# Kernel tuning notes

Measured on AMD Instinct MI355X. Metric: run time of the kernel, lower is better.

The kernel has to match this reference:

```python
import jax, jax.numpy as jnp
import numpy as np

B, S, D, L, H = 4, 2048, 1024, 2, 8  # batch, seq, d_model, hierarchy levels, heads
DH = D // H


def _ln(x, g, b, eps=1e-5):
    mu = jnp.mean(x, axis=-1, keepdims=True)
    xc = x - mu
    var = jnp.mean(xc * xc, axis=-1, keepdims=True)
    return xc * jax.lax.rsqrt(var + eps) * g + b


def setup_inputs() -> dict:
    key = jax.random.key(0)
    ks = jax.random.split(key, 16)
    s = 0.02
    f32 = jnp.float32
    return {
        "x": jax.random.normal(ks[0], (B, S, D), f32),
        "hierarchy_levels": jax.random.randint(ks[1], (B, S), 0, 3),
        # per-level processor MLPs (stacked over level axis)
        "p1_w": jax.random.normal(ks[2], (L, D, D), f32) * s,
        "p1_b": jnp.zeros((L, D), f32),
        "p2_w": jax.random.normal(ks[3], (L, D, D), f32) * s,
        "p2_b": jnp.zeros((L, D), f32),
        "ln_g": jnp.ones((L, D), f32),
        "ln_b": jnp.zeros((L, D), f32),
        # multihead attention projections
        "wq": jax.random.normal(ks[4], (D, D), f32) * s,
        "bq": jnp.zeros((D,), f32),
        "wk": jax.random.normal(ks[5], (D, D), f32) * s,
        "bk": jnp.zeros((D,), f32),
        "wv": jax.random.normal(ks[6], (D, D), f32) * s,
        "bv": jnp.zeros((D,), f32),
        "wo": jax.random.normal(ks[7], (D, D), f32) * s,
        "bo": jnp.zeros((D,), f32),
        # integration MLP: Linear(L*D -> D), SiLU, Linear(D -> D), LayerNorm
        "i1_w": jax.random.normal(ks[8], (L * D, D), f32) * s,
        "i1_b": jnp.zeros((D,), f32),
        "i2_w": jax.random.normal(ks[9], (D, D), f32) * s,
        "i2_b": jnp.zeros((D,), f32),
        "iln_g": jnp.ones((D,), f32),
        "iln_b": jnp.zeros((D,), f32),
    }


def reference(x, hierarchy_levels, p1_w, p1_b, p2_w, p2_b, ln_g, ln_b,
              wq, bq, wk, bk, wv, bv, wo, bo,
              i1_w, i1_b, i2_w, i2_b, iln_g, iln_b):
    # --- per-token expert routing: compute all L processors, select by level ---
    t = jax.nn.silu(jnp.einsum('bsd,lde->lbse', x, p1_w) + p1_b[:, None, None, :])
    h = jnp.einsum('lbse,led->lbsd', t, p2_w) + p2_b[:, None, None, :]
    h = _ln(h, ln_g[:, None, None, :], ln_b[:, None, None, :])  # [L,B,S,D]
    oh = jax.nn.one_hot(hierarchy_levels, L, dtype=x.dtype)      # [B,S,L]; level>=L -> all-zero row
    hsel = jnp.einsum('lbsd,bsl->bsd', h, oh)                    # [B,S,D]
    # --- self-attention over routed outputs ---
    q = (hsel @ wq + bq).reshape(B, S, H, DH)
    k = (hsel @ wk + bk).reshape(B, S, H, DH)
    v = (hsel @ wv + bv).reshape(B, S, H, DH)
    scores = jnp.einsum('bqhd,bkhd->bhqk', q, k) / np.sqrt(DH).astype(x.dtype)
    a = jax.nn.softmax(scores, axis=-1)                          # [B,H,S,S]
    ctx = jnp.einsum('bhqk,bkhd->bqhd', a, v).reshape(B, S, D)
    attended = ctx @ wo + bo
    attn_weights = jnp.mean(a, axis=1)                           # torch avg over heads: [B,S,S]
    # --- integration MLP ---
    z = jnp.concatenate([hsel, attended], axis=-1)               # [B,S,2D]
    z = jax.nn.silu(z @ i1_w + i1_b) @ i2_w + i2_b
    out = _ln(z, iln_g, iln_b)
    return out, attn_weights
```

## Files before the change

### kernel.cpp

```cpp
#include <hip/hip_runtime.h>
#include <cstdint>
#include <cstddef>

#define B_ 4
#define S_ 2048
#define D_ 1024
#define H_ 8
#define DH_ 128
#define MTOT 8192
#define NT_ 32
#define SCALE2 (0.08838834764831845f * 1.4426950408889634f)

typedef __attribute__((ext_vector_type(8))) short s16x8;
typedef __attribute__((ext_vector_type(4))) float f32x4;
typedef __attribute__((ext_vector_type(8))) __bf16 bf16x8;

static __device__ __forceinline__ f32x4 mfma16(s16x8 a, s16x8 b, f32x4 c) {
  return __builtin_amdgcn_mfma_f32_16x16x32_bf16(
      __builtin_bit_cast(bf16x8, a), __builtin_bit_cast(bf16x8, b), c, 0, 0, 0);
}
static __device__ __forceinline__ unsigned short f2bf(float f) {
  unsigned u = __builtin_bit_cast(unsigned, f);
  u += 0x7fffu + ((u >> 16) & 1u);
  return (unsigned short)(u >> 16);
}
static __device__ __forceinline__ float bf2f(unsigned short u) {
  return __builtin_bit_cast(float, (unsigned)u << 16);
}
static __device__ __forceinline__ unsigned cvtpk2(float a, float b) {
  unsigned r;
  asm("v_cvt_pk_bf16_f32 %0, %1, %2" : "=v"(r) : "v"(a), "v"(b));
  return r;
}
static __device__ __forceinline__ void gload_lds16(const void* g, void* l) {
  __builtin_amdgcn_global_load_lds(
      (__attribute__((address_space(1))) void*)(void*)(g),
      (__attribute__((address_space(3))) void*)(l), 16, 0, 0);
}

__global__ __launch_bounds__(256) void xconv_kernel(const float* __restrict__ x,
                                                    unsigned short* __restrict__ xb) {
  long i = ((long)blockIdx.x * 256 + threadIdx.x) * 4;
  float4 v = *(const float4*)(x + i);
  ushort4 o;
  o.x = f2bf(v.x); o.y = f2bf(v.y); o.z = f2bf(v.z); o.w = f2bf(v.w);
  *(ushort4*)(xb + i) = o;
}

__global__ __launch_bounds__(256) void route_kernel(const int* __restrict__ levels,
                                                    int* __restrict__ cnt,
                                                    int* __restrict__ ridx) {
  int row = blockIdx.x * 256 + threadIdx.x;
  int lvl = levels[row];
  if (lvl < 2) {
    int slot = atomicAdd(&cnt[lvl], 1);
    ridx[lvl * MTOT + slot] = row;
  }
}

struct WtDesc { const float* src; unsigned short* dst; long dst_ld; long dst_off; };
struct WtArgs { WtDesc d[10]; };
__global__ __launch_bounds__(256) void wtrans_all_kernel(WtArgs a) {
  __shared__ unsigned short tile[32][33];
  const int wi = blockIdx.y >> 5;
  const WtDesc de = a.d[wi];
  int r0 = (blockIdx.y & 31) * 32, c0 = blockIdx.x * 32;
  int tr = threadIdx.x >> 5, tc = threadIdx.x & 31;
#pragma unroll
  for (int i = 0; i < 4; i++)
    tile[tr + i * 8][tc] = f2bf(de.src[(long)(r0 + tr + i * 8) * 1024 + c0 + tc]);
  __syncthreads();
#pragma unroll
  for (int i = 0; i < 4; i++)
    de.dst[(long)(c0 + tr + i * 8) * de.dst_ld + de.dst_off + r0 + tc] = tile[tc][tr + i * 8];
}

__global__ __launch_bounds__(256) void vtrans_kernel(const unsigned short* __restrict__ V,
                                                     unsigned short* __restrict__ Vt) {
  __shared__ unsigned short tile[32][33];
  int b = blockIdx.z;
  int h = blockIdx.y >> 2, d0 = (blockIdx.y & 3) * 32;
  int s0 = blockIdx.x * 32;
  int tr = threadIdx.x >> 5, tc = threadIdx.x & 31;
#pragma unroll
  for (int i = 0; i < 4; i++)
    tile[tr + i * 8][tc] = V[((long)(b * S_) + s0 + tr + i * 8) * D_ + h * DH_ + d0 + tc];
  __syncthreads();
  const int sk = s0 + tc;
  const int k6 = sk & 63;
  const int slot = ((k6 >> 5) << 5) | (((k6 >> 2) & 3) << 3) | (((k6 >> 4) & 1) << 2) | (k6 & 3);
  const int ss = (sk & ~63) | slot;
#pragma unroll
  for (int i = 0; i < 4; i++)
    Vt[((long)(b * H_ + h) * DH_ + d0 + tr + i * 8) * S_ + ss] = tile[tc][tr + i * 8];
}

template <int TAG>
__global__ __launch_bounds__(256) void gemm_kernel(
    const unsigned short* __restrict__ A, int lda,
    const unsigned short* __restrict__ Wt, int ldw,
    const float* __restrict__ bias, float oscale,
    unsigned short* __restrict__ Cb, float* __restrict__ Cf, int ldc,
    int K, int do_silu) {
  __shared__ unsigned short lA[128 * 64];
  __shared__ unsigned short lB[128 * 64];
  const int t = threadIdx.x;
  const int wid = t >> 6, lane = t & 63;
  const int g = lane >> 4, lc = lane & 15;
  const int wr = wid >> 1, wc = wid & 1;
  const int nwg = gridDim.x * gridDim.y;
  int flat = blockIdx.x + gridDim.x * blockIdx.y;
  flat = (flat & 7) * (nwg >> 3) + (flat >> 3);
  const int m0 = (flat / gridDim.x) * 128;
  const int n0 = (flat % gridDim.x) * 128;
  const int srow = lane >> 3, scol = lane & 7;
  const int sxor = (scol ^ srow) << 4;

  f32x4 acc[4][4];
#pragma unroll
  for (int i = 0; i < 4; i++)
#pragma unroll
    for (int j = 0; j < 4; j++) acc[i][j] = (f32x4){0.f, 0.f, 0.f, 0.f};

  const int nk = K >> 6;
  for (int kt = 0; kt < nk; ++kt) {
    const int k0 = kt << 6;
#pragma unroll
    for (int i = 0; i < 4; i++) {
      const int r0 = wid * 32 + i * 8;
      gload_lds16((const char*)(A + (m0 + r0 + srow) * (long)lda + k0) + sxor,
                  (char*)lA + r0 * 128);
      gload_lds16((const char*)(Wt + (n0 + r0 + srow) * (long)ldw + k0) + sxor,
                  (char*)lB + r0 * 128);
    }
    __syncthreads();
#pragma unroll
    for (int kk = 0; kk < 2; kk++) {
      s16x8 af[4], bfr[4];
#pragma unroll
      for (int i = 0; i < 4; i++) {
        int row = wr * 64 + i * 16 + lc;
        af[i] = *(const s16x8*)((const char*)lA + row * 128 +
                                ((kk * 64 + g * 16) ^ ((row & 7) << 4)));
      }
#pragma unroll
      for (int j = 0; j < 4; j++) {
        int row = wc * 64 + j * 16 + lc;
        bfr[j] = *(const s16x8*)((const char*)lB + row * 128 +
                                 ((kk * 64 + g * 16) ^ ((row & 7) << 4)));
      }
#pragma unroll
      for (int i = 0; i < 4; i++)
#pragma unroll
        for (int j = 0; j < 4; j++) acc[i][j] = mfma16(af[i], bfr[j], acc[i][j]);
    }
    __syncthreads();
  }
#pragma unroll
  for (int i = 0; i < 4; i++) {
    const long rbase = m0 + wr * 64 + i * 16 + g * 4;
#pragma unroll
    for (int j = 0; j < 4; j++) {
      const int col = n0 + wc * 64 + j * 16 + lc;
      const float bv = bias[col];
#pragma unroll
      for (int r = 0; r < 4; r++) {
        float v = (acc[i][j][r] + bv) * oscale;
        if (do_silu) v = v / (1.f + __expf(-v));
        if (Cb) Cb[(rbase + r) * (long)ldc + col] = f2bf(v);
        else Cf[(rbase + r) * (long)ldc + col] = v;
      }
    }
  }
}

template <int TAG>
__global__ __launch_bounds__(512) void gemm8_kernel(
    const unsigned short* __restrict__ A, int lda,
    const unsigned short* __restrict__ Wt, int ldw,
    const float* __restrict__ bias, float oscale,
    unsigned short* __restrict__ Cb, int ldc,
    int K, int do_silu) {
  __shared__ unsigned short lA[128 * 64];
  __shared__ unsigned short lB[128 * 64];
  const int t = threadIdx.x;
  const int wid = t >> 6, lane = t & 63;
  const int g = lane >> 4, lc = lane & 15;
  const int wr = wid >> 1, wc = wid & 1;
  const int nwg = gridDim.x * gridDim.y;
  int flat = blockIdx.x + gridDim.x * blockIdx.y;
  flat = (flat & 7) * (nwg >> 3) + (flat >> 3);
  const int m0 = (flat / gridDim.x) * 128;
  const int n0 = (flat % gridDim.x) * 128;
  const int srow = lane >> 3, scol = lane & 7;
  const int sxor = (scol ^ srow) << 4;

  f32x4 acc[2][4];
#pragma unroll
  for (int i = 0; i < 2; i++)
#pragma unroll
    for (int j = 0; j < 4; j++) acc[i][j] = (f32x4){0.f, 0.f, 0.f, 0.f};

  const int nk = K >> 6;
  for (int kt = 0; kt < nk; ++kt) {
    const int k0 = kt << 6;
#pragma unroll
    for (int i = 0; i < 2; i++) {
      const int r0 = wid * 16 + i * 8;
      gload_lds16((const char*)(A + (m0 + r0 + srow) * (long)lda + k0) + sxor,
                  (char*)lA + r0 * 128);
      gload_lds16((const char*)(Wt + (n0 + r0 + srow) * (long)ldw + k0) + sxor,
                  (char*)lB + r0 * 128);
    }
    __syncthreads();
#pragma unroll
    for (int kk = 0; kk < 2; kk++) {
      s16x8 af[2], bfr[4];
#pragma unroll
      for (int i = 0; i < 2; i++) {
        int row = wr * 32 + i * 16 + lc;
        af[i] = *(const s16x8*)((const char*)lA + row * 128 +
                                ((kk * 64 + g * 16) ^ ((row & 7) << 4)));
      }
#pragma unroll
      for (int j = 0; j < 4; j++) {
        int row = wc * 64 + j * 16 + lc;
        bfr[j] = *(const s16x8*)((const char*)lB + row * 128 +
                                 ((kk * 64 + g * 16) ^ ((row & 7) << 4)));
      }
#pragma unroll
      for (int i = 0; i < 2; i++)
#pragma unroll
        for (int j = 0; j < 4; j++) acc[i][j] = mfma16(af[i], bfr[j], acc[i][j]);
    }
    __syncthreads();
  }
#pragma unroll
  for (int i = 0; i < 2; i++) {
    const long rbase = m0 + wr * 32 + i * 16 + g * 4;
#pragma unroll
    for (int j = 0; j < 4; j++) {
      const int col = n0 + wc * 64 + j * 16 + lc;
      const float bv = bias[col];
#pragma unroll
      for (int r = 0; r < 4; r++) {
        float v = (acc[i][j][r] + bv) * oscale;
        if (do_silu) v = v / (1.f + __expf(-v));
        Cb[(rbase + r) * (long)ldc + col] = f2bf(v);
      }
    }
  }
}

template <int RMAP>
__global__ __launch_bounds__(512) void gemm8_moe_kernel(
    const unsigned short* __restrict__ A, int lda,
    const unsigned short* __restrict__ Wt0, int ldw,
    const float* __restrict__ bias0,
    unsigned short* __restrict__ Cb, int ldc,
    int K, int do_silu, const int* __restrict__ ridx, const int* __restrict__ cnt2) {
  __shared__ unsigned short lA[128 * 64];
  __shared__ unsigned short lB[128 * 64];
  const int t = threadIdx.x;
  const int wid = t >> 6, lane = t & 63;
  const int g = lane >> 4, lc = lane & 15;
  const int wr = wid >> 1, wc = wid & 1;
  const int nwg = gridDim.x * gridDim.y;
  int flat = blockIdx.x + gridDim.x * blockIdx.y;
  flat = (flat & 7) * (nwg >> 3) + (flat >> 3);
  const int m0 = (flat / gridDim.x) * 128;
  const int n0 = (flat % gridDim.x) * 128;
  const int lvl = m0 >> 12;
  const int lm0 = m0 & 4095;
  if (lm0 >= cnt2[lvl]) return;
  const unsigned short* Wt = Wt0 + (long)lvl * 1048576;
  const float* bias = bias0 + lvl * 1024;
  const int srow = lane >> 3, scol = lane & 7;
  const int sxor = (scol ^ srow) << 4;

  const unsigned short* abase[2];
#pragma unroll
  for (int i = 0; i < 2; i++) {
    int ar;
    if (RMAP) ar = ridx[lvl * MTOT + lm0 + wid * 16 + i * 8 + srow];
    else ar = m0 + wid * 16 + i * 8 + srow;
    abase[i] = A + (long)ar * lda;
  }

  f32x4 acc[2][4];
#pragma unroll
  for (int i = 0; i < 2; i++)
#pragma unroll
    for (int j = 0; j < 4; j++) acc[i][j] = (f32x4){0.f, 0.f, 0.f, 0.f};

  const int nk = K >> 6;
  for (int kt = 0; kt < nk; ++kt) {
    const int k0 = kt << 6;
#pragma unroll
    for (int i = 0; i < 2; i++) {
      const int r0 = wid * 16 + i * 8;
      gload_lds16((const char*)(abase[i] + k0) + sxor, (char*)lA + r0 * 128);
      gload_lds16((const char*)(Wt + (n0 + r0 + srow) * (long)ldw + k0) + sxor,
                  (char*)lB + r0 * 128);
    }
    __syncthreads();
#pragma unroll
    for (int kk = 0; kk < 2; kk++) {
      s16x8 af[2], bfr[4];
#pragma unroll
      for (int i = 0; i < 2; i++) {
        int row = wr * 32 + i * 16 + lc;
        af[i] = *(const s16x8*)((const char*)lA + row * 128 +
                                ((kk * 64 + g * 16) ^ ((row & 7) << 4)));
      }
#pragma unroll
      for (int j = 0; j < 4; j++) {
        int row = wc * 64 + j * 16 + lc;
        bfr[j] = *(const s16x8*)((const char*)lB + row * 128 +
                                 ((kk * 64 + g * 16) ^ ((row & 7) << 4)));
      }
#pragma unroll
      for (int i = 0; i < 2; i++)
#pragma unroll
        for (int j = 0; j < 4; j++) acc[i][j] = mfma16(af[i], bfr[j], acc[i][j]);
    }
    __syncthreads();
  }
#pragma unroll
  for (int i = 0; i < 2; i++) {
    const long rbase = m0 + wr * 32 + i * 16 + g * 4;
#pragma unroll
    for (int j = 0; j < 4; j++) {
      const int col = n0 + wc * 64 + j * 16 + lc;
      const float bv = bias[col];
#pragma unroll
      for (int r = 0; r < 4; r++) {
        float v = acc[i][j][r] + bv;
        if (do_silu) v = v / (1.f + __expf(-v));
        Cb[(rbase + r) * (long)ldc + col] = f2bf(v);
      }
    }
  }
}

__global__ __launch_bounds__(256) void wct_gemm_kernel(
    const unsigned short* __restrict__ A,
    const unsigned short* __restrict__ Wb,
    float* __restrict__ Cf) {
  __shared__ unsigned short lA[128 * 64];
  __shared__ unsigned short lB[128 * 64];
  const int t = threadIdx.x;
  const int wid = t >> 6, lane = t & 63;
  const int g = lane >> 4, lc = lane & 15;
  const int wr = wid >> 1, wc = wid & 1;
  const int chunk = blockIdx.y >> 3;
  const int m0 = (blockIdx.y & 7) * 128;
  const int n0 = blockIdx.x * 128;
  const unsigned short* A0 = A + chunk * 256;
  const unsigned short* W0 = Wb + chunk * 256;
  float* C0 = Cf + (long)chunk * 1048576;
  const int srow = lane >> 3, scol = lane & 7;
  const int sxor = (scol ^ srow) << 4;

  f32x4 acc[4][4];
#pragma unroll
  for (int i = 0; i < 4; i++)
#pragma unroll
    for (int j = 0; j < 4; j++) acc[i][j] = (f32x4){0.f, 0.f, 0.f, 0.f};

  for (int kt = 0; kt < 4; ++kt) {
    const int k0 = kt << 6;
#pragma unroll
    for (int i = 0; i < 4; i++) {
      const int r0 = wid * 32 + i * 8;
      gload_lds16((const char*)(A0 + (m0 + r0 + srow) * 2048L + k0) + sxor,
                  (char*)lA + r0 * 128);
      gload_lds16((const char*)(W0 + (n0 + r0 + srow) * 1024L + k0) + sxor,
                  (char*)lB + r0 * 128);
    }
    __syncthreads();
#pragma unroll
    for (int kk = 0; kk < 2; kk++) {
      s16x8 af[4], bfr[4];
#pragma unroll
      for (int i = 0; i < 4; i++) {
        int row = wr * 64 + i * 16 + lc;
        af[i] = *(const s16x8*)((const char*)lA + row * 128 +
                                ((kk * 64 + g * 16) ^ ((row & 7) << 4)));
      }
#pragma unroll
      for (int j = 0; j < 4; j++) {
        int row = wc * 64 + j * 16 + lc;
        bfr[j] = *(const s16x8*)((const char*)lB + row * 128 +
                                 ((kk * 64 + g * 16) ^ ((row & 7) << 4)));
      }
#pragma unroll
      for (int i = 0; i < 4; i++)
#pragma unroll
        for (int j = 0; j < 4; j++) acc[i][j] = mfma16(af[i], bfr[j], acc[i][j]);
    }
    __syncthreads();
  }
#pragma unroll
  for (int i = 0; i < 4; i++) {
    const long rbase = m0 + wr * 64 + i * 16 + g * 4;
#pragma unroll
    for (int j = 0; j < 4; j++) {
      const int col = n0 + wc * 64 + j * 16 + lc;
#pragma unroll
      for (int r = 0; r < 4; r++) C0[(rbase + r) * 1024L + col] = acc[i][j][r];
    }
  }
}

__global__ __launch_bounds__(256) void wct_reduce_kernel(
    const float* __restrict__ hraw, unsigned short* __restrict__ i1t) {
  long e = ((long)blockIdx.x * 256 + threadIdx.x) * 2;
  float a0 = hraw[e] + hraw[e + 1048576] + hraw[e + 2097152] + hraw[e + 3145728];
  float a1 = hraw[e + 1] + hraw[e + 1 + 1048576] + hraw[e + 1 + 2097152] +
             hraw[e + 1 + 3145728];
  unsigned pk = cvtpk2(a0, a1);
  long n = e >> 10, c = e & 1023;
  *(unsigned*)(i1t + n * 2048 + 1024 + c) = pk;
}

__global__ __launch_bounds__(256) void biascomb_kernel(
    const unsigned short* __restrict__ i1t, const float* __restrict__ bo,
    const float* __restrict__ i1b, float* __restrict__ bias_c) {
  const int n = blockIdx.x, t = threadIdx.x;
  ushort4 w = *(const ushort4*)(i1t + (long)n * 2048 + 1024 + t * 4);
  float4 b = *(const float4*)(bo + t * 4);
  float s = bf2f(w.x) * b.x + bf2f(w.y) * b.y + bf2f(w.z) * b.z + bf2f(w.w) * b.w;
#pragma unroll
  for (int m = 32; m; m >>= 1) s += __shfl_xor(s, m);
  __shared__ float ws_[4];
  if ((t & 63) == 0) ws_[t >> 6] = s;
  __syncthreads();
  if (t == 0) bias_c[n] = i1b[n] + ws_[0] + ws_[1] + ws_[2] + ws_[3];
}

__global__ __launch_bounds__(256) void ln_moe_kernel(
    const unsigned short* __restrict__ in, const int* __restrict__ ridx,
    const int* __restrict__ cnt2,
    const float* __restrict__ gg0, const float* __restrict__ bb0,
    unsigned short* __restrict__ outb, long ldo) {
  const int row = blockIdx.x;
  const int lvl = row >> 12;
  const int lrow = row & 4095;
  if (lrow >= cnt2[lvl]) return;
  const int orow = ridx[lvl * MTOT + lrow];
  const float* gg = gg0 + lvl * 1024;
  const float* bb = bb0 + lvl * 1024;
  const int t = threadIdx.x;
  const ushort4 u = *(const ushort4*)(in + (long)row * D_ + t * 4);
  float v0 = bf2f(u.x), v1 = bf2f(u.y), v2 = bf2f(u.z), v3 = bf2f(u.w);
  float s1 = v0 + v1 + v2 + v3;
  float s2 = v0 * v0 + v1 * v1 + v2 * v2 + v3 * v3;
#pragma unroll
  for (int m = 32; m; m >>= 1) {
    s1 += __shfl_xor(s1, m);
    s2 += __shfl_xor(s2, m);
  }
  __shared__ float w1[4], w2[4];
  if ((t & 63) == 0) { w1[t >> 6] = s1; w2[t >> 6] = s2; }
  __syncthreads();
  s1 = w1[0] + w1[1] + w1[2] + w1[3];
  s2 = w2[0] + w2[1] + w2[2] + w2[3];
  const float mu = s1 * (1.f / D_);
  const float var = s2 * (1.f / D_) - mu * mu;
  const float rs = rsqrtf(var + 1e-5f);
  float vv[4] = {v0, v1, v2, v3};
#pragma unroll
  for (int jj = 0; jj < 4; jj++) {
    int col = t * 4 + jj;
    float y = (vv[jj] - mu) * rs * gg[col] + bb[col];
    outb[(long)orow * ldo + col] = f2bf(y);
  }
}

__global__ __launch_bounds__(256) void ln_kernel(
    const unsigned short* __restrict__ in,
    const float* __restrict__ gg, const float* __restrict__ bb,
    float* __restrict__ outf) {
  const int row = blockIdx.x;
  const int t = threadIdx.x;
  const ushort4 u = *(const ushort4*)(in + (long)row * D_ + t * 4);
  float v0 = bf2f(u.x), v1 = bf2f(u.y), v2 = bf2f(u.z), v3 = bf2f(u.w);
  float s1 = v0 + v1 + v2 + v3;
  float s2 = v0 * v0 + v1 * v1 + v2 * v2 + v3 * v3;
#pragma unroll
  for (int m = 32; m; m >>= 1) {
    s1 += __shfl_xor(s1, m);
    s2 += __shfl_xor(s2, m);
  }
  __shared__ float w1[4], w2[4];
  if ((t & 63) == 0) { w1[t >> 6] = s1; w2[t >> 6] = s2; }
  __syncthreads();
  s1 = w1[0] + w1[1] + w1[2] + w1[3];
  s2 = w2[0] + w2[1] + w2[2] + w2[3];
  const float mu = s1 * (1.f / D_);
  const float var = s2 * (1.f / D_) - mu * mu;
  const float rs = rsqrtf(var + 1e-5f);
  float vv[4] = {v0, v1, v2, v3};
#pragma unroll
  for (int jj = 0; jj < 4; jj++) {
    int col = t * 4 + jj;
    outf[(long)row * D_ + col] = (vv[jj] - mu) * rs * gg[col] + bb[col];
  }
}

__global__ __launch_bounds__(256) void gemm_qkv_kernel(
    const unsigned short* __restrict__ A, int lda,
    const unsigned short* __restrict__ Wt,
    const float* __restrict__ bq, const float* __restrict__ bk,
    const float* __restrict__ bv,
    unsigned short* __restrict__ qb, unsigned short* __restrict__ kb,
    unsigned short* __restrict__ vb) {
  __shared__ unsigned short lA[128 * 64];
  __shared__ unsigned short lB[128 * 64];
  const int t = threadIdx.x;
  const int wid = t >> 6, lane = t & 63;
  const int g = lane >> 4, lc = lane & 15;
  const int wr = wid >> 1, wc = wid & 1;
  const int nwg = gridDim.x * gridDim.y;
  int flat = blockIdx.x + gridDim.x * blockIdx.y;
  flat = (flat & 7) * (nwg >> 3) + (flat >> 3);
  const int m0 = (flat / gridDim.x) * 128;
  const int n0 = (flat % gridDim.x) * 128;
  const int srow = lane >> 3, scol = lane & 7;
  const int sxor = (scol ^ srow) << 4;

  f32x4 acc[4][4];
#pragma unroll
  for (int i = 0; i < 4; i++)
#pragma unroll
    for (int j = 0; j < 4; j++) acc[i][j] = (f32x4){0.f, 0.f, 0.f, 0.f};

  for (int kt = 0; kt < 16; ++kt) {
    const int k0 = kt << 6;
#pragma unroll
    for (int i = 0; i < 4; i++) {
      const int r0 = wid * 32 + i * 8;
      gload_lds16((const char*)(A + (m0 + r0 + srow) * (long)lda + k0) + sxor,
                  (char*)lA + r0 * 128);
      gload_lds16((const char*)(Wt + (n0 + r0 + srow) * 1024 + k0) + sxor,
                  (char*)lB + r0 * 128);
    }
    __syncthreads();
#pragma unroll
    for (int kk = 0; kk < 2; kk++) {
      s16x8 af[4], bfr[4];
#pragma unroll
      for (int i = 0; i < 4; i++) {
        int row = wr * 64 + i * 16 + lc;
        af[i] = *(const s16x8*)((const char*)lA + row * 128 +
                                ((kk * 64 + g * 16) ^ ((row & 7) << 4)));
      }
#pragma unroll
      for (int j = 0; j < 4; j++) {
        int row = wc * 64 + j * 16 + lc;
        bfr[j] = *(const s16x8*)((const char*)lB + row * 128 +
                                 ((kk * 64 + g * 16) ^ ((row & 7) << 4)));
      }
#pragma unroll
      for (int i = 0; i < 4; i++)
#pragma unroll
        for (int j = 0; j < 4; j++) acc[i][j] = mfma16(af[i], bfr[j], acc[i][j]);
    }
    __syncthreads();
  }
  const int whichB = n0 >> 10;
  const float* bias = whichB == 0 ? bq : whichB == 1 ? bk : bv;
  unsigned short* Cb = whichB == 0 ? qb : whichB == 1 ? kb : vb;
  const float oscale = whichB == 0 ? (float)SCALE2 : 1.0f;
  const int nb = n0 & 1023;
#pragma unroll
  for (int i = 0; i < 4; i++) {
    const long rbase = m0 + wr * 64 + i * 16 + g * 4;
#pragma unroll
    for (int j = 0; j < 4; j++) {
      const int col = nb + wc * 64 + j * 16 + lc;
      const float bvv = bias[col];
#pragma unroll
      for (int r = 0; r < 4; r++) {
        float v = (acc[i][j][r] + bvv) * oscale;
        Cb[(rbase + r) * 1024L + col] = f2bf(v);
      }
    }
  }
}

__global__ __launch_bounds__(256, 2) void flash_kernel(
    const unsigned short* __restrict__ Q, const unsigned short* __restrict__ Kb,
    const unsigned short* __restrict__ Vt,
    unsigned short* __restrict__ zatt, float* __restrict__ Mo, float* __restrict__ Lo) {
  __shared__ unsigned short lK[2][64 * 128];
  __shared__ unsigned short lV[2][128 * 64];
  const int t = threadIdx.x, wid = t >> 6, lane = t & 63;
  const int g = lane >> 4, lc = lane & 15;
  const int d = blockIdx.x + 16 * (blockIdx.y + 8 * blockIdx.z);
  const int qd = d >> 3, rd = d & 7;
  const int grp = rd + 8 * (qd >> 4);
  const int b = grp >> 3, h = grp & 7, q0 = (qd & 15) * 128;
  const int k_l4 = lane >> 4, k_c = lane & 15;
  const int v_l3 = lane >> 3, v_c = lane & 7;

  s16x8 qf[2][4];
#pragma unroll
  for (int qi = 0; qi < 2; qi++)
#pragma unroll
    for (int kk = 0; kk < 4; kk++)
      qf[qi][kk] = *(const s16x8*)(Q +
          ((long)(b * S_ + q0 + wid * 32 + qi * 16 + lc)) * D_ + h * DH_ + kk * 32 + g * 8);

  f32x4 acco[2][8];
#pragma unroll
  for (int qi = 0; qi < 2; qi++)
#pragma unroll
    for (int dn = 0; dn < 8; dn++) acco[qi][dn] = (f32x4){0.f, 0.f, 0.f, 0.f};
  float m_run[2] = {-1e30f, -1e30f}, l_run[2] = {0.f, 0.f};

  auto stageK = [&](int kt, int buf) {
#pragma unroll
    for (int i = 0; i < 4; i++) {
      const int r0 = wid * 16 + i * 4;
      const int row = r0 + k_l4;
      gload_lds16((const char*)(Kb + (b * S_ + kt * 64 + row) * D_ + h * DH_) +
                      ((k_c ^ (row & 7)) << 4),
                  (char*)&lK[buf][0] + r0 * 256);
    }
  };
  auto stageV = [&](int kt, int buf) {
#pragma unroll
    for (int i = 0; i < 4; i++) {
      const int r0 = wid * 32 + i * 8;
      const int row = r0 + v_l3;
      gload_lds16((const char*)(Vt + ((b * H_ + h) * DH_ + row) * S_ + kt * 64) +
                      ((v_c ^ (row & 7)) << 4),
                  (char*)&lV[buf][0] + r0 * 128);
    }
  };

  stageK(0, 0);
  stageV(0, 0);
  __syncthreads();

  for (int kt = 0; kt < NT_; ++kt) {
    const int cur = kt & 1;
    if (kt + 1 < NT_) { stageK(kt + 1, cur ^ 1); stageV(kt + 1, cur ^ 1); }

    f32x4 s[2][4];
#pragma unroll
    for (int qi = 0; qi < 2; qi++)
#pragma unroll
      for (int kn = 0; kn < 4; kn++) s[qi][kn] = (f32x4){0.f, 0.f, 0.f, 0.f};
    __builtin_amdgcn_s_setprio(1);
#pragma unroll
    for (int kk = 0; kk < 4; kk++) {
      s16x8 kf[4];
#pragma unroll
      for (int kn = 0; kn < 4; kn++) {
        int row = kn * 16 + lc;
        kf[kn] = *(const s16x8*)((const char*)&lK[cur][0] + row * 256 +
                                 ((kk * 64 + g * 16) ^ ((row & 7) << 4)));
      }
#pragma unroll
      for (int qi = 0; qi < 2; qi++)
#pragma unroll
        for (int kn = 0; kn < 4; kn++) s[qi][kn] = mfma16(kf[kn], qf[qi][kk], s[qi][kn]);
    }
    __builtin_amdgcn_s_setprio(0);

    float mx[2];
    int trig = 0;
#pragma unroll
    for (int qi = 0; qi < 2; qi++) {
      float m01 = fmaxf(fmaxf(s[qi][0][0], s[qi][0][1]), fmaxf(s[qi][0][2], s[qi][0][3]));
      float m1 = fmaxf(fmaxf(s[qi][1][0], s[qi][1][1]), fmaxf(s[qi][1][2], s[qi][1][3]));
      float m2 = fmaxf(fmaxf(s[qi][2][0], s[qi][2][1]), fmaxf(s[qi][2][2], s[qi][2][3]));
      float m3 = fmaxf(fmaxf(s[qi][3][0], s[qi][3][1]), fmaxf(s[qi][3][2], s[qi][3][3]));
      float m = fmaxf(fmaxf(m01, m1), fmaxf(m2, m3));
      m = fmaxf(m, __shfl_xor(m, 16));
      m = fmaxf(m, __shfl_xor(m, 32));
      mx[qi] = m;
      trig |= (m > m_run[qi] + 8.0f);
    }
    if (__any(trig)) {
#pragma unroll
      for (int qi = 0; qi < 2; qi++) {
        float mn = fmaxf(m_run[qi], mx[qi]);
        float fsc = exp2f(m_run[qi] - mn);
        m_run[qi] = mn;
        l_run[qi] *= fsc;
#pragma unroll
        for (int dn = 0; dn < 8; dn++)
#pragma unroll
          for (int r = 0; r < 4; r++) acco[qi][dn][r] *= fsc;
      }
    }

    unsigned w[2][4][2];
#pragma unroll
    for (int qi = 0; qi < 2; qi++) {
      float ls = 0.f;
#pragma unroll
      for (int kn = 0; kn < 4; kn++) {
        float p0 = exp2f(s[qi][kn][0] - m_run[qi]);
        float p1 = exp2f(s[qi][kn][1] - m_run[qi]);
        float p2 = exp2f(s[qi][kn][2] - m_run[qi]);
        float p3 = exp2f(s[qi][kn][3] - m_run[qi]);
        ls += (p0 + p1) + (p2 + p3);
        w[qi][kn][0] = cvtpk2(p0, p1);
        w[qi][kn][1] = cvtpk2(p2, p3);
      }
      ls += __shfl_xor(ls, 16);
      ls += __shfl_xor(ls, 32);
      l_run[qi] += ls;
    }

    __builtin_amdgcn_s_setprio(1);
#pragma unroll
    for (int kk = 0; kk < 2; kk++) {
      s16x8 pf[2];
#pragma unroll
      for (int qi = 0; qi < 2; qi++) {
        union { unsigned u[4]; s16x8 v; } pu;
        pu.u[0] = w[qi][2 * kk][0];
        pu.u[1] = w[qi][2 * kk][1];
        pu.u[2] = w[qi][2 * kk + 1][0];
        pu.u[3] = w[qi][2 * kk + 1][1];
        pf[qi] = pu.v;
      }
#pragma unroll
      for (int dn = 0; dn < 8; dn++) {
        int vrow = dn * 16 + lc;
        s16x8 vf = *(const s16x8*)((const char*)&lV[cur][0] + vrow * 128 +
                                   ((kk * 64 + g * 16) ^ ((vrow & 7) << 4)));
#pragma unroll
        for (int qi = 0; qi < 2; qi++) acco[qi][dn] = mfma16(vf, pf[qi], acco[qi][dn]);
      }
    }
    __builtin_amdgcn_s_setprio(0);
    __syncthreads();
  }

  char* tb = (char*)&lK[0][0] + wid * 8192;
#pragma unroll
  for (int qi = 0; qi < 2; qi++) {
    float inv = 1.f / l_run[qi];
    int row = qi * 16 + lc;
#pragma unroll
    for (int dn = 0; dn < 8; dn++) {
      unsigned lo = cvtpk2(acco[qi][dn][0] * inv, acco[qi][dn][1] * inv);
      unsigned hi = cvtpk2(acco[qi][dn][2] * inv, acco[qi][dn][3] * inv);
      unsigned long long pk = (unsigned long long)lo | ((unsigned long long)hi << 32);
      *(unsigned long long*)(tb + row * 256 + ((dn * 32 + g * 8) ^ ((row & 7) << 4))) = pk;
    }
  }
  __syncthreads();
#pragma unroll
  for (int i = 0; i < 8; i++) {
    const int row = i * 4 + (lane >> 4);
    const int chunk = lane & 15;
    s16x8 vv = *(const s16x8*)(tb + row * 256 + ((chunk * 16) ^ ((row & 7) << 4)));
    *(s16x8*)(zatt + ((long)(b * S_ + q0 + wid * 32 + row)) * 2048 + h * DH_ + chunk * 8) = vv;
  }
  if (g == 0) {
#pragma unroll
    for (int qi = 0; qi < 2; qi++) {
      int q = q0 + wid * 32 + qi * 16 + lc;
      Mo[(long)(b * H_ + h) * S_ + q] = m_run[qi];
      Lo[(long)(b * H_ + h) * S_ + q] = l_run[qi];
    }
  }
}

__global__ __launch_bounds__(256) void attw_kernel(
    const unsigned short* __restrict__ Q, const unsigned short* __restrict__ Kb,
    const float* __restrict__ Mo, const float* __restrict__ Lo,
    float* __restrict__ AW) {
  __shared__ unsigned short lK[2][128 * 128];
  __shared__ float lm[H_][128], winv[H_][128];
  const int t = threadIdx.x, wid = t >> 6, lane = t & 63;
  const int g = lane >> 4, lc = lane & 15;
  const int f = blockIdx.x + 16 * (blockIdx.y + 16 * blockIdx.z);
  const int xcd = f & 7, i_ = f >> 3;
  const int grp = (i_ >> 4) * 8 + xcd;
  const int b = grp >> 4, k0 = (grp & 15) * 128, q0 = (i_ & 15) * 128;
  const int k_l4 = lane >> 4, k_c = lane & 15;

  for (int i = t; i < H_ * 128; i += 256) {
    int h = i >> 7, qq = i & 127;
    lm[h][qq] = Mo[(long)(b * H_ + h) * S_ + q0 + qq];
    winv[h][qq] = 0.125f / Lo[(long)(b * H_ + h) * S_ + q0 + qq];
  }

  auto stageK = [&](int h, int buf) {
#pragma unroll
    for (int i = 0; i < 8; i++) {
      const int r0 = wid * 32 + i * 4;
      const int row = r0 + k_l4;
      gload_lds16((const char*)(Kb + ((long)(b * S_ + k0 + row)) * D_ + h * DH_) +
                      ((k_c ^ (row & 7)) << 4),
                  (char*)&lK[buf][0] + r0 * 256);
    }
  };

  f32x4 acc[2][8];
#pragma unroll
  for (int qi = 0; qi < 2; qi++)
#pragma unroll
    for (int kn = 0; kn < 8; kn++) acc[qi][kn] = (f32x4){0.f, 0.f, 0.f, 0.f};

  stageK(0, 0);
  __syncthreads();

  for (int h = 0; h < H_; ++h) {
    const int cur = h & 1;
    if (h + 1 < H_) stageK(h + 1, cur ^ 1);
    f32x4 s[2][8];
#pragma unroll
    for (int qi = 0; qi < 2; qi++)
#pragma unroll
      for (int kn = 0; kn < 8; kn++) s[qi][kn] = (f32x4){0.f, 0.f, 0.f, 0.f};
    __builtin_amdgcn_s_setprio(1);
#pragma unroll
    for (int kk = 0; kk < 4; kk++) {
      s16x8 qa[2];
#pragma unroll
      for (int qi = 0; qi < 2; qi++)
        qa[qi] = *(const s16x8*)(Q +
            ((long)(b * S_ + q0 + wid * 32 + qi * 16 + lc)) * D_ + h * DH_ + kk * 32 + g * 8);
#pragma unroll
      for (int kn = 0; kn < 8; kn++) {
        int row = kn * 16 + lc;
        s16x8 kf = *(const s16x8*)((const char*)&lK[cur][0] + row * 256 +
                                   ((kk * 64 + g * 16) ^ ((row & 7) << 4)));
#pragma unroll
        for (int qi = 0; qi < 2; qi++) s[qi][kn] = mfma16(qa[qi], kf, s[qi][kn]);
      }
    }
    __builtin_amdgcn_s_setprio(0);
#pragma unroll
    for (int qi = 0; qi < 2; qi++)
#pragma unroll
      for (int kn = 0; kn < 8; kn++)
#pragma unroll
        for (int r = 0; r < 4; r++) {
          int qq = wid * 32 + qi * 16 + g * 4 + r;
          acc[qi][kn][r] += exp2f(s[qi][kn][r] - lm[h][qq]) * winv[h][qq];
        }
    __syncthreads();
  }
#pragma unroll
  for (int qi = 0; qi < 2; qi++)
#pragma unroll
    for (int kn = 0; kn < 8; kn++)
#pragma unroll
      for (int r = 0; r < 4; r++) {
        long q = q0 + wid * 32 + qi * 16 + g * 4 + r;
        int k = k0 + kn * 16 + lc;
        AW[((long)b * S_ + q) * S_ + k] = acc[qi][kn][r];
      }
}

__global__ void signal_kernel(float* out, float v) { out[0] = v; }

extern "C" void kernel_launch(void* const* d_in, const int* in_sizes, int n_in,
                              void* d_out, int out_size, void* d_ws, size_t ws_size,
                              hipStream_t stream) {
  constexpr size_t OFF_XB = 0;
  constexpr size_t OFF_W = 16777216ULL;
  constexpr size_t OFF_T = 39845888ULL;
  constexpr size_t OFF_HR = 56623104ULL;
  constexpr size_t OFF_Z = 90177536ULL;
  constexpr size_t OFF_Q = 123731968ULL;
  constexpr size_t OFF_K = 140509184ULL;
  constexpr size_t OFF_V = 157286400ULL;
  constexpr size_t OFF_VT = 174063616ULL;
  constexpr size_t OFF_M = 190840832ULL;
  constexpr size_t OFF_L = 191102976ULL;
  constexpr size_t OFF_CNT = 191365120ULL;
  constexpr size_t OFF_RIDX = 191365184ULL;
  constexpr size_t OFF_BC = OFF_RIDX + 2ULL * MTOT * 4;
  constexpr size_t WS_NEED = OFF_BC + 4096;

  if (ws_size < WS_NEED) {
    signal_kernel<<<1, 1, 0, stream>>>((float*)d_out, (float)ws_size);
    return;
  }
  const float* x = (const float*)d_in[0];
  const int* levels = (const int*)d_in[1];
  const float* p1w = (const float*)d_in[2];
  const float* p1b = (const float*)d_in[3];
  const float* p2w = (const float*)d_in[4];
  const float* p2b = (const float*)d_in[5];
  const float* lng = (const float*)d_in[6];
  const float* lnb = (const float*)d_in[7];
  const float* wq = (const float*)d_in[8];
  const float* bq = (const float*)d_in[9];
  const float* wk = (const float*)d_in[10];
  const float* bk = (const float*)d_in[11];
  const float* wv = (const float*)d_in[12];
  const float* bv = (const float*)d_in[13];
  const float* wo = (const float*)d_in[14];
  const float* bo = (const float*)d_in[15];
  const float* i1w = (const float*)d_in[16];
  const float* i1b = (const float*)d_in[17];
  const float* i2w = (const float*)d_in[18];
  const float* i2b = (const float*)d_in[19];
  const float* ilng = (const float*)d_in[20];
  const float* ilnb = (const float*)d_in[21];

  char* ws = (char*)d_ws;
  unsigned short* xb = (unsigned short*)(ws + OFF_XB);
  unsigned short* p1t = (unsigned short*)(ws + OFF_W);
  unsigned short* p2t = p1t + 2 * 1048576;
  unsigned short* wqt = p2t + 2 * 1048576;
  unsigned short* wkt = wqt + 1048576;
  unsigned short* wvt = wkt + 1048576;
  unsigned short* wob = wvt + 1048576;
  unsigned short* i1t = wob + 1048576;
  unsigned short* i2t = i1t + 2097152;
  unsigned short* tbuf = (unsigned short*)(ws + OFF_T);
  float* wctp = (float*)(ws + OFF_HR);
  unsigned short* hraw16 = (unsigned short*)(ws + OFF_HR);
  unsigned short* z = (unsigned short*)(ws + OFF_Z);
  unsigned short* qb = (unsigned short*)(ws + OFF_Q);
  unsigned short* kb = (unsigned short*)(ws + OFF_K);
  unsigned short* vb = (unsigned short*)(ws + OFF_V);
  unsigned short* vt = (unsigned short*)(ws + OFF_VT);
  float* Mo = (float*)(ws + OFF_M);
  float* Lo = (float*)(ws + OFF_L);
  int* cnt = (int*)(ws + OFF_CNT);
  int* ridx = (int*)(ws + OFF_RIDX);
  float* bias_c = (float*)(ws + OFF_BC);
  float* out = (float*)d_out;
  float* aw = out + (size_t)MTOT * D_;

  dim3 blk(256), blk8(512);
  hipMemsetAsync(cnt, 0, 64, stream);
  hipMemsetAsync(ridx, 0, 2 * MTOT * 4, stream);
  xconv_kernel<<<8192, blk, 0, stream>>>(x, xb);
  route_kernel<<<32, blk, 0, stream>>>(levels, cnt, ridx);

  WtArgs wa;
  wa.d[0] = {p1w, p1t, 1024, 0};
  wa.d[1] = {p1w + 1048576, p1t + 1048576, 1024, 0};
  wa.d[2] = {p2w, p2t, 1024, 0};
  wa.d[3] = {p2w + 1048576, p2t + 1048576, 1024, 0};
  wa.d[4] = {wq, wqt, 1024, 0};
  wa.d[5] = {wk, wkt, 1024, 0};
  wa.d[6] = {wv, wvt, 1024, 0};
  wa.d[7] = {i1w, i1t, 2048, 0};
  wa.d[8] = {i1w + 1048576, i1t, 2048, 1024};
  wa.d[9] = {i2w, i2t, 1024, 0};
  wtrans_all_kernel<<<dim3(32, 320), blk, 0, stream>>>(wa);
  xconv_kernel<<<1024, blk, 0, stream>>>(wo, wob);
  wct_gemm_kernel<<<dim3(8, 32), blk, 0, stream>>>(i1t + 1024, wob, wctp);
  biascomb_kernel<<<1024, blk, 0, stream>>>(i1t, bo, i1b, bias_c);
  wct_reduce_kernel<<<2048, blk, 0, stream>>>(wctp, i1t);
  hipMemsetAsync(z, 0, 33554432, stream);

  gemm8_moe_kernel<1><<<dim3(8, 64), blk8, 0, stream>>>(xb, 1024, p1t, 1024, p1b,
                                                        tbuf, 1024, 1024, 1, ridx, cnt);
  gemm8_moe_kernel<0><<<dim3(8, 64), blk8, 0, stream>>>(tbuf, 1024, p2t, 1024, p2b,
                                                        hraw16, 1024, 1024, 0, ridx, cnt);
  ln_moe_kernel<<<8192, blk, 0, stream>>>(hraw16, ridx, cnt, lng, lnb, z, 2048);

  gemm_qkv_kernel<<<dim3(24, 64), blk, 0, stream>>>(z, 2048, wqt, bq, bk, bv, qb, kb, vb);
  vtrans_kernel<<<dim3(64, 32, 4), blk, 0, stream>>>(vb, vt);
  flash_kernel<<<dim3(16, 8, 4), blk, 0, stream>>>(qb, kb, vt, z + 1024, Mo, Lo);
  attw_kernel<<<dim3(16, 16, 4), blk, 0, stream>>>(qb, kb, Mo, Lo, aw);
  gemm8_kernel<3><<<dim3(8, 64), blk8, 0, stream>>>(z, 2048, i1t, 2048, bias_c, 1.0f, tbuf,
                                                    1024, 2048, 1);
  gemm8_kernel<4><<<dim3(8, 64), blk8, 0, stream>>>(tbuf, 1024, i2t, 1024, i2b, 1.0f, hraw16,
                                                    1024, 1024, 0);
  ln_kernel<<<8192, blk, 0, stream>>>(hraw16, ilng, ilnb, out);
}
```

Before: 472.9 us.

## Skip QKV GEMM for level-2 tokens by gathering active rows and filling bias

Routing now builds a compacted list of tokens with level<2 (active) and a list of level-2 tokens whose routed output is all zeros. The QKV GEMM gathers only active rows through the index list, scatters results back, and skips tiles past the active count. Level-2 rows get their q/k/v set directly to the (scaled) biases and their z half zeroed, which replaces the full 32MB memset of z. This cuts about a third of the QKV GEMM work on random levels, at the cost of an indirect gather and scatter and an extra launch. Partial final tiles read zero-initialized indices, so they compute row 0 and write it back redundantly.

```diff
diff --git a/kernel.cpp b/kernel.cpp
--- a/kernel.cpp
+++ b/kernel.cpp
@@ -49,13 +49,44 @@
 
 __global__ __launch_bounds__(256) void route_kernel(const int* __restrict__ levels,
                                                     int* __restrict__ cnt,
-                                                    int* __restrict__ ridx) {
+                                                    int* __restrict__ ridx,
+                                                    int* __restrict__ act,
+                                                    int* __restrict__ act2) {
   int row = blockIdx.x * 256 + threadIdx.x;
   int lvl = levels[row];
   if (lvl < 2) {
     int slot = atomicAdd(&cnt[lvl], 1);
     ridx[lvl * MTOT + slot] = row;
-  }
+    int s2 = atomicAdd(&cnt[2], 1);
+    act[s2] = row;
+  } else {
+    int s3 = atomicAdd(&cnt[3], 1);
+    act2[s3] = row;
+  }
+}
+
+__global__ __launch_bounds__(256) void lvl2fill_kernel(
+    const int* __restrict__ act2, const int* __restrict__ cntp,
+    const float* __restrict__ bq, const float* __restrict__ bk,
+    const float* __restrict__ bv,
+    unsigned short* __restrict__ qb, unsigned short* __restrict__ kb,
+    unsigned short* __restrict__ vb, unsigned short* __restrict__ z) {
+  const int idx = blockIdx.x;
+  if (idx >= *cntp) return;
+  const long row = act2[idx];
+  const int t = threadIdx.x;
+  const float4 q4 = *(const float4*)(bq + t * 4);
+  const float4 k4 = *(const float4*)(bk + t * 4);
+  const float4 v4 = *(const float4*)(bv + t * 4);
+  ushort4 qo, ko, vo;
+  qo.x = f2bf(q4.x * SCALE2); qo.y = f2bf(q4.y * SCALE2);
+  qo.z = f2bf(q4.z * SCALE2); qo.w = f2bf(q4.w * SCALE2);
+  ko.x = f2bf(k4.x); ko.y = f2bf(k4.y); ko.z = f2bf(k4.z); ko.w = f2bf(k4.w);
+  vo.x = f2bf(v4.x); vo.y = f2bf(v4.y); vo.z = f2bf(v4.z); vo.w = f2bf(v4.w);
+  *(ushort4*)(qb + row * 1024 + t * 4) = qo;
+  *(ushort4*)(kb + row * 1024 + t * 4) = ko;
+  *(ushort4*)(vb + row * 1024 + t * 4) = vo;
+  *(ushort4*)(z + row * 2048 + t * 4) = (ushort4){0, 0, 0, 0};
 }
 
 struct WtDesc { const float* src; unsigned short* dst; long dst_ld; long dst_off; };
@@ -515,7 +546,8 @@
     const float* __restrict__ bq, const float* __restrict__ bk,
     const float* __restrict__ bv,
     unsigned short* __restrict__ qb, unsigned short* __restrict__ kb,
-    unsigned short* __restrict__ vb) {
+    unsigned short* __restrict__ vb,
+    const int* __restrict__ act, const int* __restrict__ cntp) {
   __shared__ unsigned short lA[128 * 64];
   __shared__ unsigned short lB[128 * 64];
   const int t = threadIdx.x;
@@ -527,9 +559,15 @@
   flat = (flat & 7) * (nwg >> 3) + (flat >> 3);
   const int m0 = (flat / gridDim.x) * 128;
   const int n0 = (flat % gridDim.x) * 128;
+  if (m0 >= *cntp) return;
   const int srow = lane >> 3, scol = lane & 7;
   const int sxor = (scol ^ srow) << 4;
 
+  const unsigned short* abase[4];
+#pragma unroll
+  for (int i = 0; i < 4; i++)
+    abase[i] = A + (long)act[m0 + wid * 32 + i * 8 + srow] * lda;
+
   f32x4 acc[4][4];
 #pragma unroll
   for (int i = 0; i < 4; i++)
@@ -541,8 +579,7 @@
 #pragma unroll
     for (int i = 0; i < 4; i++) {
       const int r0 = wid * 32 + i * 8;
-      gload_lds16((const char*)(A + (m0 + r0 + srow) * (long)lda + k0) + sxor,
-                  (char*)lA + r0 * 128);
+      gload_lds16((const char*)(abase[i] + k0) + sxor, (char*)lA + r0 * 128);
       gload_lds16((const char*)(Wt + (n0 + r0 + srow) * 1024 + k0) + sxor,
                   (char*)lB + r0 * 128);
     }
@@ -576,7 +613,7 @@
   const int nb = n0 & 1023;
 #pragma unroll
   for (int i = 0; i < 4; i++) {
-    const long rbase = m0 + wr * 64 + i * 16 + g * 4;
+    const int ribase = m0 + wr * 64 + i * 16 + g * 4;
 #pragma unroll
     for (int j = 0; j < 4; j++) {
       const int col = nb + wc * 64 + j * 16 + lc;
@@ -584,7 +621,7 @@
 #pragma unroll
       for (int r = 0; r < 4; r++) {
         float v = (acc[i][j][r] + bvv) * oscale;
-        Cb[(rbase + r) * 1024L + col] = f2bf(v);
+        Cb[(long)act[ribase + r] * 1024L + col] = f2bf(v);
       }
     }
   }
@@ -883,7 +920,9 @@
   constexpr size_t OFF_CNT = 191365120ULL;
   constexpr size_t OFF_RIDX = 191365184ULL;
   constexpr size_t OFF_BC = OFF_RIDX + 2ULL * MTOT * 4;
-  constexpr size_t WS_NEED = OFF_BC + 4096;
+  constexpr size_t OFF_ACT = OFF_BC + 4096;
+  constexpr size_t OFF_ACT2 = OFF_ACT + MTOT * 4;
+  constexpr size_t WS_NEED = OFF_ACT2 + MTOT * 4;
 
   if (ws_size < WS_NEED) {
     signal_kernel<<<1, 1, 0, stream>>>((float*)d_out, (float)ws_size);
@@ -935,14 +974,18 @@
   int* cnt = (int*)(ws + OFF_CNT);
   int* ridx = (int*)(ws + OFF_RIDX);
   float* bias_c = (float*)(ws + OFF_BC);
+  int* act = (int*)(ws + OFF_ACT);
+  int* act2 = (int*)(ws + OFF_ACT2);
   float* out = (float*)d_out;
   float* aw = out + (size_t)MTOT * D_;
 
   dim3 blk(256), blk8(512);
   hipMemsetAsync(cnt, 0, 64, stream);
   hipMemsetAsync(ridx, 0, 2 * MTOT * 4, stream);
+  hipMemsetAsync(act, 0, MTOT * 4, stream);
   xconv_kernel<<<8192, blk, 0, stream>>>(x, xb);
-  route_kernel<<<32, blk, 0, stream>>>(levels, cnt, ridx);
+  route_kernel<<<32, blk, 0, stream>>>(levels, cnt, ridx, act, act2);
+  lvl2fill_kernel<<<MTOT, blk, 0, stream>>>(act2, cnt + 3, bq, bk, bv, qb, kb, vb, z);
 
   WtArgs wa;
   wa.d[0] = {p1w, p1t, 1024, 0};
@@ -960,7 +1003,6 @@
   wct_gemm_kernel<<<dim3(8, 32), blk, 0, stream>>>(i1t + 1024, wob, wctp);
   biascomb_kernel<<<1024, blk, 0, stream>>>(i1t, bo, i1b, bias_c);
   wct_reduce_kernel<<<2048, blk, 0, stream>>>(wctp, i1t);
-  hipMemsetAsync(z, 0, 33554432, stream);
 
   gemm8_moe_kernel<1><<<dim3(8, 64), blk8, 0, stream>>>(xb, 1024, p1t, 1024, p1b,
                                                         tbuf, 1024, 1024, 1, ridx, cnt);
@@ -968,7 +1010,8 @@
                                                         hraw16, 1024, 1024, 0, ridx, cnt);
   ln_moe_kernel<<<8192, blk, 0, stream>>>(hraw16, ridx, cnt, lng, lnb, z, 2048);
 
-  gemm_qkv_kernel<<<dim3(24, 64), blk, 0, stream>>>(z, 2048, wqt, bq, bk, bv, qb, kb, vb);
+  gemm_qkv_kernel<<<dim3(24, 64), blk, 0, stream>>>(z, 2048, wqt, bq, bk, bv, qb, kb, vb,
+                                                    act, cnt + 2);
   vtrans_kernel<<<dim3(64, 32, 4), blk, 0, stream>>>(vb, vt);
   flash_kernel<<<dim3(16, 8, 4), blk, 0, stream>>>(qb, kb, vt, z + 1024, Mo, Lo);
   attw_kernel<<<dim3(16, 16, 4), blk, 0, stream>>>(qb, kb, Mo, Lo, aw);
```

Result: slower. 545.7 us (+15.4%).
